# Optimization experiments

Hardware: AMD Instinct MI355X
Metric: run time of the kernel (lower is better)

Reference implementation:

```python
import math
import jax, jax.numpy as jnp
import numpy as np

D_MODEL = 256
NUM_HEADS = 8
HEAD_DIM = D_MODEL // NUM_HEADS
B, S = 4, 2048


def setup_inputs() -> dict:
    key = jax.random.key(0)
    ks = jax.random.split(key, 12)
    scale = 1.0 / math.sqrt(D_MODEL)
    inp = {
        "query": jax.random.normal(ks[0], (B, S, D_MODEL), dtype=jnp.float32),
        "key": jax.random.normal(ks[1], (B, S, D_MODEL), dtype=jnp.float32),
        "value": jax.random.normal(ks[2], (B, S, D_MODEL), dtype=jnp.float32),
        "mask": jax.random.randint(ks[3], (B, 1, S, S), 0, 2, dtype=jnp.int32),
        # nn.Linear weights are [out_features, in_features]
        "Wq": jax.random.uniform(ks[4], (D_MODEL, D_MODEL), jnp.float32, -scale, scale),
        "bq": jnp.zeros((D_MODEL,), jnp.float32),
        "Wk": jax.random.uniform(ks[5], (D_MODEL, D_MODEL), jnp.float32, -scale, scale),
        "bk": jnp.zeros((D_MODEL,), jnp.float32),
        "Wv": jax.random.uniform(ks[6], (D_MODEL, D_MODEL), jnp.float32, -scale, scale),
        "bv": jnp.zeros((D_MODEL,), jnp.float32),
        "Wo": jax.random.uniform(ks[7], (D_MODEL, D_MODEL), jnp.float32, -scale, scale),
        "bo": jnp.zeros((D_MODEL,), jnp.float32),
    }
    return inp


def _split_heads(x):
    # [B, S, d_model] -> [B, H, S, head_dim]
    b, s, _ = x.shape
    return x.reshape(b, s, NUM_HEADS, HEAD_DIM).transpose(0, 2, 1, 3)


def reference(query, key, value, mask, Wq, bq, Wk, bk, Wv, bv, Wo, bo):
    q = _split_heads(query @ Wq.T + bq)
    k = _split_heads(key @ Wk.T + bk)
    v = _split_heads(value @ Wv.T + bv)
    energy = jnp.einsum("bhqd,bhkd->bhqk", q, k)  # [B, H, S, S]
    # masked_fill(mask == 0, -inf), then scale AFTER masking (as in the source)
    energy = jnp.where(mask == 0, -jnp.inf, energy)
    attn = jax.nn.softmax(energy / math.sqrt(HEAD_DIM), axis=-1)
    out = jnp.einsum("bhqk,bhkd->bhqd", attn, v)  # [B, H, S, head_dim]
    b = out.shape[0]
    out = out.transpose(0, 2, 1, 3).reshape(b, -1, D_MODEL)
    return out @ Wo.T + bo
```

## Files before the change

### kernel.cpp

```cpp
#include <hip/hip_runtime.h>
#include <stdint.h>

#define D_MODEL 256
#define NHEAD   8
#define HDIM    32
#define BATCH   4
#define SEQ     2048
#define MTOT    (BATCH*SEQ)

typedef float f32x4 __attribute__((ext_vector_type(4)));
typedef short s16x8 __attribute__((ext_vector_type(8)));

__device__ __forceinline__ unsigned short f2bf(float f) {
    union { float f; uint32_t u; } v; v.f = f;
    uint32_t u = v.u;
    u += 0x7fffu + ((u >> 16) & 1u);
    return (unsigned short)(u >> 16);
}

__device__ __forceinline__ uint32_t cvtpk_bf16(float a, float b) {
    uint32_t r;
    asm("v_cvt_pk_bf16_f32 %0, %1, %2" : "=v"(r) : "v"(a), "v"(b));
    return r;
}

__global__ __launch_bounds__(256)
void prep(const float* __restrict__ q, const float* __restrict__ k, const float* __restrict__ v,
          const float* __restrict__ wq, const float* __restrict__ wk,
          const float* __restrict__ wv, const float* __restrict__ wo,
          unsigned short* __restrict__ qb, unsigned short* __restrict__ kb,
          unsigned short* __restrict__ vb,
          unsigned short* __restrict__ wqb, unsigned short* __restrict__ wkb,
          unsigned short* __restrict__ wvb, unsigned short* __restrict__ wob, float csc) {
    const int y = blockIdx.y;
    const float* src; unsigned short* dst; int n; float sc = 1.0f;
    switch (y) {
        case 0:  src = q;  dst = qb;  n = MTOT * 256; break;
        case 1:  src = k;  dst = kb;  n = MTOT * 256; break;
        case 2:  src = v;  dst = vb;  n = MTOT * 256; break;
        case 3:  src = wq; dst = wqb; n = 65536; sc = csc; break;
        case 4:  src = wk; dst = wkb; n = 65536; break;
        case 5:  src = wv; dst = wvb; n = 65536; break;
        default: src = wo; dst = wob; n = 65536; break;
    }
    const int i = (blockIdx.x * 256 + threadIdx.x) * 4;
    if (i >= n) return;
    f32x4 x = *(const f32x4*)(src + i);
    ushort4 o;
    o.x = f2bf(x[0] * sc); o.y = f2bf(x[1] * sc);
    o.z = f2bf(x[2] * sc); o.w = f2bf(x[3] * sc);
    *(ushort4*)(dst + i) = o;
}

__global__ void pack_mask(const int* __restrict__ mask,
                          unsigned long long* __restrict__ pm) {
    const int lane = threadIdx.x & 63;
    const int wid  = (blockIdx.x * blockDim.x + threadIdx.x) >> 6;
    const int nw   = (gridDim.x * blockDim.x) >> 6;
    const int nchunks = BATCH * SEQ * (SEQ / 64);
    for (int c = wid; c < nchunks; c += nw) {
        int v = mask[(size_t)c * 64 + lane];
        unsigned long long bits = __ballot(v != 0);
        if (lane == 0) pm[c] = bits;
    }
}

__global__ __launch_bounds__(256, 3)
void proj3(const unsigned short* __restrict__ Xq, const unsigned short* __restrict__ Xk,
           const unsigned short* __restrict__ Xv,
           const unsigned short* __restrict__ Wqb, const unsigned short* __restrict__ Wkb,
           const unsigned short* __restrict__ Wvb,
           const float* __restrict__ bq, const float* __restrict__ bk,
           const float* __restrict__ bv,
           unsigned short* __restrict__ Qh, unsigned short* __restrict__ Kh,
           unsigned short* __restrict__ Vt, float csc) {
    const int y = blockIdx.y;
    const unsigned short* X = (y == 0) ? Xq : (y == 1) ? Xk : Xv;
    const unsigned short* W = (y == 0) ? Wqb : (y == 1) ? Wkb : Wvb;
    const float* bias = (y == 0) ? bq : (y == 1) ? bk : bv;
    const float bscale = (y == 0) ? csc : 1.0f;

    const int t = threadIdx.x, lane = t & 63, w = t >> 6;
    const int fr = lane & 15, fg = lane >> 4;
    const int m0 = blockIdx.x * 32;
    const int n0w = w * 64;

    f32x4 acc[2][4] = {};

    if (y < 2) {
        #pragma unroll 2
        for (int k0 = 0; k0 < 256; k0 += 32) {
            s16x8 xf[2], wf[4];
            #pragma unroll
            for (int mg = 0; mg < 2; ++mg)
                xf[mg] = *(const s16x8*)(X + ((size_t)(m0 + mg*16 + fr) << 8) + k0 + (fg << 3));
            #pragma unroll
            for (int ng = 0; ng < 4; ++ng)
                wf[ng] = *(const s16x8*)(W + ((size_t)(n0w + ng*16 + fr) << 8) + k0 + (fg << 3));
            #pragma unroll
            for (int mg = 0; mg < 2; ++mg)
                #pragma unroll
                for (int ng = 0; ng < 4; ++ng)
                    acc[mg][ng] = __builtin_amdgcn_mfma_f32_16x16x32_bf16(
                        wf[ng], xf[mg], acc[mg][ng], 0, 0, 0);
        }
        unsigned short* OUT = (y == 0) ? Qh : Kh;
        #pragma unroll
        for (int mg = 0; mg < 2; ++mg) {
            const int m = m0 + mg*16 + fr;
            const int bb = m >> 11, ss = m & 2047;
            #pragma unroll
            for (int ng = 0; ng < 4; ++ng) {
                const int nb = n0w + ng*16 + fg*4;
                const int hh = nb >> 5, db = nb & 31;
                f32x4 bi = *(const f32x4*)(bias + nb);
                ushort4 o;
                o.x = f2bf(acc[mg][ng][0] + bi[0] * bscale);
                o.y = f2bf(acc[mg][ng][1] + bi[1] * bscale);
                o.z = f2bf(acc[mg][ng][2] + bi[2] * bscale);
                o.w = f2bf(acc[mg][ng][3] + bi[3] * bscale);
                *(ushort4*)(OUT + (((size_t)(bb*8 + hh) * SEQ) + ss) * 32 + db) = o;
            }
        }
    } else {
        #pragma unroll 2
        for (int k0 = 0; k0 < 256; k0 += 32) {
            s16x8 xf[2], wf[4];
            #pragma unroll
            for (int mg = 0; mg < 2; ++mg)
                xf[mg] = *(const s16x8*)(X + ((size_t)(m0 + mg*16 + fr) << 8) + k0 + (fg << 3));
            #pragma unroll
            for (int ng = 0; ng < 4; ++ng)
                wf[ng] = *(const s16x8*)(W + ((size_t)(n0w + ng*16 + fr) << 8) + k0 + (fg << 3));
            #pragma unroll
            for (int mg = 0; mg < 2; ++mg)
                #pragma unroll
                for (int ng = 0; ng < 4; ++ng)
                    acc[mg][ng] = __builtin_amdgcn_mfma_f32_16x16x32_bf16(
                        xf[mg], wf[ng], acc[mg][ng], 0, 0, 0);
        }
        #pragma unroll
        for (int mg = 0; mg < 2; ++mg) {
            const int sb = m0 + mg*16 + fg*4;
            const int bb = sb >> 11, ss = sb & 2047;
            #pragma unroll
            for (int ng = 0; ng < 4; ++ng) {
                const int n = n0w + ng*16 + fr;
                const int hh = n >> 5, dd = n & 31;
                const float bi = bias[n];
                ushort4 o;
                o.x = f2bf(acc[mg][ng][0] + bi);
                o.y = f2bf(acc[mg][ng][1] + bi);
                o.z = f2bf(acc[mg][ng][2] + bi);
                o.w = f2bf(acc[mg][ng][3] + bi);
                *(ushort4*)(Vt + (((size_t)(bb*8 + hh) * 32) + dd) * SEQ + ss) = o;
            }
        }
    }
}

__global__ __launch_bounds__(256, 3)
void oproj(const unsigned short* __restrict__ Ao, const unsigned short* __restrict__ Wo,
           const float* __restrict__ bo, float* __restrict__ out) {
    const int t = threadIdx.x, lane = t & 63, w = t >> 6;
    const int fr = lane & 15, fg = lane >> 4;
    const int m0 = blockIdx.x * 32;
    const int n0w = w * 64;

    f32x4 acc[2][4] = {};
    #pragma unroll 2
    for (int k0 = 0; k0 < 256; k0 += 32) {
        s16x8 xf[2], wf[4];
        #pragma unroll
        for (int mg = 0; mg < 2; ++mg)
            xf[mg] = *(const s16x8*)(Ao + ((size_t)(m0 + mg*16 + fr) << 8) + k0 + (fg << 3));
        #pragma unroll
        for (int ng = 0; ng < 4; ++ng)
            wf[ng] = *(const s16x8*)(Wo + ((size_t)(n0w + ng*16 + fr) << 8) + k0 + (fg << 3));
        #pragma unroll
        for (int mg = 0; mg < 2; ++mg)
            #pragma unroll
            for (int ng = 0; ng < 4; ++ng)
                acc[mg][ng] = __builtin_amdgcn_mfma_f32_16x16x32_bf16(
                    wf[ng], xf[mg], acc[mg][ng], 0, 0, 0);
    }
    #pragma unroll
    for (int mg = 0; mg < 2; ++mg) {
        const int m = m0 + mg*16 + fr;
        #pragma unroll
        for (int ng = 0; ng < 4; ++ng) {
            const int nb = n0w + ng*16 + fg*4;
            f32x4 bi = *(const f32x4*)(bo + nb);
            f32x4 vv = acc[mg][ng] + bi;
            *(f32x4*)(out + (size_t)m * 256 + nb) = vv;
        }
    }
}

struct TR {
    s16x8 kf[4];
    s16x8 vf[2][2];
    unsigned long long mw[2];
};

__device__ __forceinline__ void load_tile(TR& tr, int ti,
        const unsigned short* Kb, const unsigned short* Vb,
        const unsigned long long* pm0, const unsigned long long* pm1,
        int fr, int fg) {
    tr.mw[0] = pm0[ti];
    tr.mw[1] = pm1[ti];
    #pragma unroll
    for (int g = 0; g < 4; ++g)
        tr.kf[g] = *(const s16x8*)(Kb + ((ti*64 + g*16 + fr) << 5) + (fg << 3));
    #pragma unroll
    for (int c = 0; c < 2; ++c)
        #pragma unroll
        for (int hh = 0; hh < 2; ++hh)
            tr.vf[c][hh] = *(const s16x8*)(Vb + ((hh*16 + fr) << 11) + ti*64 + c*32 + (fg << 3));
}

__device__ __forceinline__ void compute_tile(const TR& tr, const s16x8* qf,
        f32x4 acc[2][2], float* mrun, float* lrun, char* ptb, int fr, int fg) {
    #pragma unroll
    for (int j = 0; j < 2; ++j) {
        const unsigned long long wsh = tr.mw[j] >> (fg * 4);
        const uint32_t wlo = (uint32_t)wsh, whi = (uint32_t)(wsh >> 32);
        f32x4 s[4];
        #pragma unroll
        for (int g = 0; g < 4; ++g) {
            const uint32_t wsel = (g < 2) ? wlo : whi;
            f32x4 cm;
            #pragma unroll
            for (int r = 0; r < 4; ++r)
                cm[r] = ((wsel >> ((g & 1) * 16 + r)) & 1u) ? 0.0f : -1.0e30f;
            s[g] = __builtin_amdgcn_mfma_f32_16x16x32_bf16(tr.kf[g], qf[j], cm, 0, 0, 0);
        }
        float v[16];
        #pragma unroll
        for (int g = 0; g < 4; ++g)
            #pragma unroll
            for (int r = 0; r < 4; ++r)
                v[g*4 + r] = s[g][r];
        float t8[8];
        #pragma unroll
        for (int i = 0; i < 8; ++i) t8[i] = fmaxf(v[2*i], v[2*i+1]);
        float mx = fmaxf(fmaxf(fmaxf(t8[0], t8[1]), fmaxf(t8[2], t8[3])),
                         fmaxf(fmaxf(t8[4], t8[5]), fmaxf(t8[6], t8[7])));
        mx = fmaxf(mx, __shfl_xor(mx, 16));
        mx = fmaxf(mx, __shfl_xor(mx, 32));
        const float mn = fmaxf(mrun[j], mx);
        const float rs = exp2f(mrun[j] - mn);
        mrun[j] = mn;
        float p[16];
        #pragma unroll
        for (int i = 0; i < 16; ++i) p[i] = exp2f(v[i] - mn);
        float s8[8];
        #pragma unroll
        for (int i = 0; i < 8; ++i) s8[i] = p[2*i] + p[2*i+1];
        float sum = ((s8[0]+s8[1]) + (s8[2]+s8[3])) + ((s8[4]+s8[5]) + (s8[6]+s8[7]));
        sum += __shfl_xor(sum, 16);
        sum += __shfl_xor(sum, 32);
        lrun[j] = lrun[j] * rs + sum;
        acc[j][0] *= rs;
        acc[j][1] *= rs;
        char* row = ptb + (j << 11) + fr * 128;
        #pragma unroll
        for (int g = 0; g < 4; ++g) {
            const uint32_t p0 = cvtpk_bf16(p[g*4+0], p[g*4+1]);
            const uint32_t p1 = cvtpk_bf16(p[g*4+2], p[g*4+3]);
            const int slot = (g*2 + (fg >> 1)) ^ (fr & 7);
            *(uint2*)(row + (slot << 4) + ((fg & 1) << 3)) = make_uint2(p0, p1);
        }
        #pragma unroll
        for (int c = 0; c < 2; ++c) {
            const int slot = (c*4 + fg) ^ (fr & 7);
            const s16x8 pb = *(const s16x8*)(row + (slot << 4));
            #pragma unroll
            for (int hh = 0; hh < 2; ++hh)
                acc[j][hh] = __builtin_amdgcn_mfma_f32_16x16x32_bf16(
                    tr.vf[c][hh], pb, acc[j][hh], 0, 0, 0);
        }
    }
}

__global__ __launch_bounds__(256, 2)
void attn_fused(const unsigned short* __restrict__ Qh,
                const unsigned short* __restrict__ Kh,
                const unsigned short* __restrict__ Vt,
                const unsigned long long* __restrict__ pm,
                unsigned short* __restrict__ Ao) {
    __shared__ __align__(16) char ptbuf[16384];
    const int t = threadIdx.x, lane = t & 63, w = t >> 6;
    const int fr = lane & 15, fg = lane >> 4;
    const int by = blockIdx.y, b = by >> 3, h = by & 7;
    const int q0 = blockIdx.x * 128 + w * 32;
    const unsigned short* Qb = Qh + (size_t)by * SEQ * HDIM;
    const unsigned short* Kb = Kh + (size_t)by * SEQ * HDIM;
    const unsigned short* Vb = Vt + (size_t)by * HDIM * SEQ;
    const unsigned long long* pm0 = pm + ((size_t)b * SEQ + q0 + fr) * 32;
    const unsigned long long* pm1 = pm0 + 16 * 32;
    char* ptb = ptbuf + (w << 12);

    s16x8 qf[2];
    #pragma unroll
    for (int j = 0; j < 2; ++j)
        qf[j] = *(const s16x8*)(Qb + ((q0 + j*16 + fr) << 5) + (fg << 3));

    f32x4 acc[2][2] = {};
    float mrun[2] = {-1e20f, -1e20f};
    float lrun[2] = {0.0f, 0.0f};

    TR A, B;
    load_tile(A, 0, Kb, Vb, pm0, pm1, fr, fg);
    #pragma unroll 1
    for (int ti = 0; ti < 32; ti += 2) {
        load_tile(B, ti + 1, Kb, Vb, pm0, pm1, fr, fg);
        compute_tile(A, qf, acc, mrun, lrun, ptb, fr, fg);
        load_tile(A, (ti + 2 < 32) ? ti + 2 : 31, Kb, Vb, pm0, pm1, fr, fg);
        compute_tile(B, qf, acc, mrun, lrun, ptb, fr, fg);
    }

    #pragma unroll
    for (int j = 0; j < 2; ++j) {
        const float inv = 1.0f / lrun[j];
        const int q = q0 + j*16 + fr;
        #pragma unroll
        for (int hh = 0; hh < 2; ++hh) {
            ushort4 o;
            o.x = f2bf(acc[j][hh][0] * inv);
            o.y = f2bf(acc[j][hh][1] * inv);
            o.z = f2bf(acc[j][hh][2] * inv);
            o.w = f2bf(acc[j][hh][3] * inv);
            *(ushort4*)(Ao + (((size_t)b * SEQ + q) * 8 + h) * 32 + hh*16 + fg*4) = o;
        }
    }
}

extern "C" void kernel_launch(void* const* d_in, const int* in_sizes, int n_in,
                              void* d_out, int out_size, void* d_ws, size_t ws_size,
                              hipStream_t stream) {
    const float* query = (const float*)d_in[0];
    const float* key   = (const float*)d_in[1];
    const float* value = (const float*)d_in[2];
    const int*   mask  = (const int*)  d_in[3];
    const float* Wq = (const float*)d_in[4];   const float* bq = (const float*)d_in[5];
    const float* Wk = (const float*)d_in[6];   const float* bk = (const float*)d_in[7];
    const float* Wv = (const float*)d_in[8];   const float* bv = (const float*)d_in[9];
    const float* Wo = (const float*)d_in[10];  const float* bo = (const float*)d_in[11];

    char* ws = (char*)d_ws;
    const size_t MB = 1024 * 1024;
    unsigned short* qbf = (unsigned short*)(ws);
    unsigned short* kbf = (unsigned short*)(ws + 4*MB);
    unsigned short* vbf = (unsigned short*)(ws + 8*MB);
    unsigned short* wqb = (unsigned short*)(ws + 12*MB);
    unsigned short* wkb = (unsigned short*)(ws + 12*MB + 131072);
    unsigned short* wvb = (unsigned short*)(ws + 12*MB + 262144);
    unsigned short* wob = (unsigned short*)(ws + 12*MB + 393216);
    unsigned long long* pmw = (unsigned long long*)(ws + 12*MB + 524288);
    unsigned short* Qh = (unsigned short*)(ws + 14*MB + 524288);
    unsigned short* Kh = (unsigned short*)(ws + 18*MB + 524288);
    unsigned short* Vt = (unsigned short*)(ws + 22*MB + 524288);
    unsigned short* Aob = (unsigned short*)(ws);

    const float csc = (float)(0.17677669529663687 * 1.4426950408889634);

    prep<<<dim3(2048, 7), 256, 0, stream>>>(query, key, value, Wq, Wk, Wv, Wo,
                                            qbf, kbf, vbf, wqb, wkb, wvb, wob, csc);
    pack_mask<<<2048, 256, 0, stream>>>(mask, pmw);
    proj3<<<dim3(256, 3), 256, 0, stream>>>(qbf, kbf, vbf, wqb, wkb, wvb,
                                            bq, bk, bv, Qh, Kh, Vt, csc);
    attn_fused<<<dim3(16, 32), 256, 0, stream>>>(Qh, Kh, Vt, pmw, Aob);
    oproj<<<dim3(256), 256, 0, stream>>>(Aob, wob, bo, (float*)d_out);
}
```

Baseline: 243.7 us.

## Fuse fp32-to-bf16 conversion into projections, split-K attention with combine, lazy rescale

The separate prep conversion kernel is removed, and the projection GEMMs now load fp32 inputs and weights and convert them to bf16 in registers. Attention is split along the key dimension into two partitions, doubling the grid. Each partition writes unnormalised fp32 partial outputs plus its running max and sum, and a new combine kernel merges them. Inside the softmax, the mask is applied after exponentiation instead of as an MFMA bias, and the online max rescale only runs when the new max exceeds the old one by more than a threshold. This trades one extra kernel and fp32 partial traffic for more parallelism and fewer full-size conversion passes, at some numerical risk from the lazy-rescale threshold.

```diff
diff --git a/kernel.cpp b/kernel.cpp
--- a/kernel.cpp
+++ b/kernel.cpp
@@ -24,32 +24,15 @@
     return r;
 }
 
-__global__ __launch_bounds__(256)
-void prep(const float* __restrict__ q, const float* __restrict__ k, const float* __restrict__ v,
-          const float* __restrict__ wq, const float* __restrict__ wk,
-          const float* __restrict__ wv, const float* __restrict__ wo,
-          unsigned short* __restrict__ qb, unsigned short* __restrict__ kb,
-          unsigned short* __restrict__ vb,
-          unsigned short* __restrict__ wqb, unsigned short* __restrict__ wkb,
-          unsigned short* __restrict__ wvb, unsigned short* __restrict__ wob, float csc) {
-    const int y = blockIdx.y;
-    const float* src; unsigned short* dst; int n; float sc = 1.0f;
-    switch (y) {
-        case 0:  src = q;  dst = qb;  n = MTOT * 256; break;
-        case 1:  src = k;  dst = kb;  n = MTOT * 256; break;
-        case 2:  src = v;  dst = vb;  n = MTOT * 256; break;
-        case 3:  src = wq; dst = wqb; n = 65536; sc = csc; break;
-        case 4:  src = wk; dst = wkb; n = 65536; break;
-        case 5:  src = wv; dst = wvb; n = 65536; break;
-        default: src = wo; dst = wob; n = 65536; break;
-    }
-    const int i = (blockIdx.x * 256 + threadIdx.x) * 4;
-    if (i >= n) return;
-    f32x4 x = *(const f32x4*)(src + i);
-    ushort4 o;
-    o.x = f2bf(x[0] * sc); o.y = f2bf(x[1] * sc);
-    o.z = f2bf(x[2] * sc); o.w = f2bf(x[3] * sc);
-    *(ushort4*)(dst + i) = o;
+__device__ __forceinline__ s16x8 ldfrag_f32(const float* p) {
+    f32x4 a = *(const f32x4*)p;
+    f32x4 b = *(const f32x4*)(p + 4);
+    union { uint32_t u[4]; s16x8 v; } r;
+    r.u[0] = cvtpk_bf16(a[0], a[1]);
+    r.u[1] = cvtpk_bf16(a[2], a[3]);
+    r.u[2] = cvtpk_bf16(b[0], b[1]);
+    r.u[3] = cvtpk_bf16(b[2], b[3]);
+    return r.v;
 }
 
 __global__ void pack_mask(const int* __restrict__ mask,
@@ -66,19 +49,19 @@
 }
 
 __global__ __launch_bounds__(256, 3)
-void proj3(const unsigned short* __restrict__ Xq, const unsigned short* __restrict__ Xk,
-           const unsigned short* __restrict__ Xv,
-           const unsigned short* __restrict__ Wqb, const unsigned short* __restrict__ Wkb,
-           const unsigned short* __restrict__ Wvb,
+void proj3(const float* __restrict__ Xq, const float* __restrict__ Xk,
+           const float* __restrict__ Xv,
+           const float* __restrict__ Wq, const float* __restrict__ Wk,
+           const float* __restrict__ Wv,
            const float* __restrict__ bq, const float* __restrict__ bk,
            const float* __restrict__ bv,
            unsigned short* __restrict__ Qh, unsigned short* __restrict__ Kh,
            unsigned short* __restrict__ Vt, float csc) {
     const int y = blockIdx.y;
-    const unsigned short* X = (y == 0) ? Xq : (y == 1) ? Xk : Xv;
-    const unsigned short* W = (y == 0) ? Wqb : (y == 1) ? Wkb : Wvb;
+    const float* X = (y == 0) ? Xq : (y == 1) ? Xk : Xv;
+    const float* W = (y == 0) ? Wq : (y == 1) ? Wk : Wv;
     const float* bias = (y == 0) ? bq : (y == 1) ? bk : bv;
-    const float bscale = (y == 0) ? csc : 1.0f;
+    const float sc = (y == 0) ? csc : 1.0f;
 
     const int t = threadIdx.x, lane = t & 63, w = t >> 6;
     const int fr = lane & 15, fg = lane >> 4;
@@ -93,10 +76,10 @@
             s16x8 xf[2], wf[4];
             #pragma unroll
             for (int mg = 0; mg < 2; ++mg)
-                xf[mg] = *(const s16x8*)(X + ((size_t)(m0 + mg*16 + fr) << 8) + k0 + (fg << 3));
+                xf[mg] = ldfrag_f32(X + ((size_t)(m0 + mg*16 + fr) << 8) + k0 + (fg << 3));
             #pragma unroll
             for (int ng = 0; ng < 4; ++ng)
-                wf[ng] = *(const s16x8*)(W + ((size_t)(n0w + ng*16 + fr) << 8) + k0 + (fg << 3));
+                wf[ng] = ldfrag_f32(W + ((size_t)(n0w + ng*16 + fr) << 8) + k0 + (fg << 3));
             #pragma unroll
             for (int mg = 0; mg < 2; ++mg)
                 #pragma unroll
@@ -115,10 +98,10 @@
                 const int hh = nb >> 5, db = nb & 31;
                 f32x4 bi = *(const f32x4*)(bias + nb);
                 ushort4 o;
-                o.x = f2bf(acc[mg][ng][0] + bi[0] * bscale);
-                o.y = f2bf(acc[mg][ng][1] + bi[1] * bscale);
-                o.z = f2bf(acc[mg][ng][2] + bi[2] * bscale);
-                o.w = f2bf(acc[mg][ng][3] + bi[3] * bscale);
+                o.x = f2bf((acc[mg][ng][0] + bi[0]) * sc);
+                o.y = f2bf((acc[mg][ng][1] + bi[1]) * sc);
+                o.z = f2bf((acc[mg][ng][2] + bi[2]) * sc);
+                o.w = f2bf((acc[mg][ng][3] + bi[3]) * sc);
                 *(ushort4*)(OUT + (((size_t)(bb*8 + hh) * SEQ) + ss) * 32 + db) = o;
             }
         }
@@ -128,10 +111,10 @@
             s16x8 xf[2], wf[4];
             #pragma unroll
             for (int mg = 0; mg < 2; ++mg)
-                xf[mg] = *(const s16x8*)(X + ((size_t)(m0 + mg*16 + fr) << 8) + k0 + (fg << 3));
+                xf[mg] = ldfrag_f32(X + ((size_t)(m0 + mg*16 + fr) << 8) + k0 + (fg << 3));
             #pragma unroll
             for (int ng = 0; ng < 4; ++ng)
-                wf[ng] = *(const s16x8*)(W + ((size_t)(n0w + ng*16 + fr) << 8) + k0 + (fg << 3));
+                wf[ng] = ldfrag_f32(W + ((size_t)(n0w + ng*16 + fr) << 8) + k0 + (fg << 3));
             #pragma unroll
             for (int mg = 0; mg < 2; ++mg)
                 #pragma unroll
@@ -160,7 +143,7 @@
 }
 
 __global__ __launch_bounds__(256, 3)
-void oproj(const unsigned short* __restrict__ Ao, const unsigned short* __restrict__ Wo,
+void oproj(const unsigned short* __restrict__ Ao, const float* __restrict__ Wo,
            const float* __restrict__ bo, float* __restrict__ out) {
     const int t = threadIdx.x, lane = t & 63, w = t >> 6;
     const int fr = lane & 15, fg = lane >> 4;
@@ -176,7 +159,7 @@
             xf[mg] = *(const s16x8*)(Ao + ((size_t)(m0 + mg*16 + fr) << 8) + k0 + (fg << 3));
         #pragma unroll
         for (int ng = 0; ng < 4; ++ng)
-            wf[ng] = *(const s16x8*)(Wo + ((size_t)(n0w + ng*16 + fr) << 8) + k0 + (fg << 3));
+            wf[ng] = ldfrag_f32(Wo + ((size_t)(n0w + ng*16 + fr) << 8) + k0 + (fg << 3));
         #pragma unroll
         for (int mg = 0; mg < 2; ++mg)
             #pragma unroll
@@ -228,12 +211,8 @@
         f32x4 s[4];
         #pragma unroll
         for (int g = 0; g < 4; ++g) {
-            const uint32_t wsel = (g < 2) ? wlo : whi;
-            f32x4 cm;
-            #pragma unroll
-            for (int r = 0; r < 4; ++r)
-                cm[r] = ((wsel >> ((g & 1) * 16 + r)) & 1u) ? 0.0f : -1.0e30f;
-            s[g] = __builtin_amdgcn_mfma_f32_16x16x32_bf16(tr.kf[g], qf[j], cm, 0, 0, 0);
+            const f32x4 cz = {0.0f, 0.0f, 0.0f, 0.0f};
+            s[g] = __builtin_amdgcn_mfma_f32_16x16x32_bf16(tr.kf[g], qf[j], cz, 0, 0, 0);
         }
         float v[16];
         #pragma unroll
@@ -241,6 +220,11 @@
             #pragma unroll
             for (int r = 0; r < 4; ++r)
                 v[g*4 + r] = s[g][r];
+
+        float p[16];
+        #pragma unroll
+        for (int i = 0; i < 16; ++i) p[i] = exp2f(v[i] - mrun[j]);
+
         float t8[8];
         #pragma unroll
         for (int i = 0; i < 8; ++i) t8[i] = fmaxf(v[2*i], v[2*i+1]);
@@ -248,21 +232,41 @@
                          fmaxf(fmaxf(t8[4], t8[5]), fmaxf(t8[6], t8[7])));
         mx = fmaxf(mx, __shfl_xor(mx, 16));
         mx = fmaxf(mx, __shfl_xor(mx, 32));
-        const float mn = fmaxf(mrun[j], mx);
-        const float rs = exp2f(mrun[j] - mn);
-        mrun[j] = mn;
-        float p[16];
-        #pragma unroll
-        for (int i = 0; i < 16; ++i) p[i] = exp2f(v[i] - mn);
+
+        #pragma unroll
+        for (int g = 0; g < 4; ++g) {
+            const uint32_t wsel = (g < 2) ? wlo : whi;
+            #pragma unroll
+            for (int r = 0; r < 4; ++r)
+                p[g*4 + r] = ((wsel >> ((g & 1) * 16 + r)) & 1u) ? p[g*4 + r] : 0.0f;
+        }
+
+        if (!__all(mx <= mrun[j] + 8.0f)) {
+            const float mn = fmaxf(mrun[j], mx);
+            const float rs = exp2f(mrun[j] - mn);
+            #pragma unroll
+            for (int i = 0; i < 16; ++i) p[i] = exp2f(v[i] - mn);
+            #pragma unroll
+            for (int g = 0; g < 4; ++g) {
+                const uint32_t wsel = (g < 2) ? wlo : whi;
+                #pragma unroll
+                for (int r = 0; r < 4; ++r)
+                    p[g*4 + r] = ((wsel >> ((g & 1) * 16 + r)) & 1u) ? p[g*4 + r] : 0.0f;
+            }
+            mrun[j] = mn;
+            lrun[j] *= rs;
+            acc[j][0] *= rs;
+            acc[j][1] *= rs;
+        }
+
         float s8[8];
         #pragma unroll
         for (int i = 0; i < 8; ++i) s8[i] = p[2*i] + p[2*i+1];
         float sum = ((s8[0]+s8[1]) + (s8[2]+s8[3])) + ((s8[4]+s8[5]) + (s8[6]+s8[7]));
         sum += __shfl_xor(sum, 16);
         sum += __shfl_xor(sum, 32);
-        lrun[j] = lrun[j] * rs + sum;
-        acc[j][0] *= rs;
-        acc[j][1] *= rs;
+        lrun[j] += sum;
+
         char* row = ptb + (j << 11) + fr * 128;
         #pragma unroll
         for (int g = 0; g < 4; ++g) {
@@ -283,21 +287,22 @@
     }
 }
 
-__global__ __launch_bounds__(256, 2)
+__global__ __launch_bounds__(256, 4)
 void attn_fused(const unsigned short* __restrict__ Qh,
                 const unsigned short* __restrict__ Kh,
                 const unsigned short* __restrict__ Vt,
                 const unsigned long long* __restrict__ pm,
-                unsigned short* __restrict__ Ao) {
+                float* __restrict__ Opart, float2* __restrict__ MLpart) {
     __shared__ __align__(16) char ptbuf[16384];
     const int t = threadIdx.x, lane = t & 63, w = t >> 6;
     const int fr = lane & 15, fg = lane >> 4;
-    const int by = blockIdx.y, b = by >> 3, h = by & 7;
+    const int by = blockIdx.y, b = by >> 3;
+    const int kz = blockIdx.z;
     const int q0 = blockIdx.x * 128 + w * 32;
     const unsigned short* Qb = Qh + (size_t)by * SEQ * HDIM;
-    const unsigned short* Kb = Kh + (size_t)by * SEQ * HDIM;
-    const unsigned short* Vb = Vt + (size_t)by * HDIM * SEQ;
-    const unsigned long long* pm0 = pm + ((size_t)b * SEQ + q0 + fr) * 32;
+    const unsigned short* Kb = Kh + (size_t)by * SEQ * HDIM + ((size_t)kz << 15);
+    const unsigned short* Vb = Vt + (size_t)by * HDIM * SEQ + ((size_t)kz << 10);
+    const unsigned long long* pm0 = pm + ((size_t)b * SEQ + q0 + fr) * 32 + kz * 16;
     const unsigned long long* pm1 = pm0 + 16 * 32;
     char* ptb = ptbuf + (w << 12);
 
@@ -313,27 +318,45 @@
     TR A, B;
     load_tile(A, 0, Kb, Vb, pm0, pm1, fr, fg);
     #pragma unroll 1
-    for (int ti = 0; ti < 32; ti += 2) {
+    for (int ti = 0; ti < 16; ti += 2) {
         load_tile(B, ti + 1, Kb, Vb, pm0, pm1, fr, fg);
         compute_tile(A, qf, acc, mrun, lrun, ptb, fr, fg);
-        load_tile(A, (ti + 2 < 32) ? ti + 2 : 31, Kb, Vb, pm0, pm1, fr, fg);
+        load_tile(A, (ti + 2 < 16) ? ti + 2 : 15, Kb, Vb, pm0, pm1, fr, fg);
         compute_tile(B, qf, acc, mrun, lrun, ptb, fr, fg);
     }
 
     #pragma unroll
     for (int j = 0; j < 2; ++j) {
-        const float inv = 1.0f / lrun[j];
         const int q = q0 + j*16 + fr;
-        #pragma unroll
-        for (int hh = 0; hh < 2; ++hh) {
-            ushort4 o;
-            o.x = f2bf(acc[j][hh][0] * inv);
-            o.y = f2bf(acc[j][hh][1] * inv);
-            o.z = f2bf(acc[j][hh][2] * inv);
-            o.w = f2bf(acc[j][hh][3] * inv);
-            *(ushort4*)(Ao + (((size_t)b * SEQ + q) * 8 + h) * 32 + hh*16 + fg*4) = o;
-        }
-    }
+        const size_t row = ((size_t)(kz*32 + by) * SEQ) + q;
+        #pragma unroll
+        for (int hh = 0; hh < 2; ++hh)
+            *(f32x4*)(Opart + row * 32 + hh*16 + fg*4) = acc[j][hh];
+        if (fg == 0)
+            MLpart[row] = make_float2(mrun[j], lrun[j]);
+    }
+}
+
+__global__ __launch_bounds__(256)
+void combine(const float* __restrict__ Opart, const float2* __restrict__ ML,
+             unsigned short* __restrict__ Ao) {
+    const int t = blockIdx.x * 256 + threadIdx.x;
+    const int row = t >> 3, c = t & 7;
+    const float2 ml1 = ML[row];
+    const float2 ml2 = ML[row + 65536];
+    const float m = fmaxf(ml1.x, ml2.x);
+    const float w1 = exp2f(ml1.x - m), w2 = exp2f(ml2.x - m);
+    const float inv = 1.0f / (w1 * ml1.y + w2 * ml2.y);
+    const f32x4 o1 = *(const f32x4*)(Opart + (size_t)row * 32 + c * 4);
+    const f32x4 o2 = *(const f32x4*)(Opart + ((size_t)row + 65536) * 32 + c * 4);
+    const int bh = row >> 11, q = row & 2047;
+    const int b = bh >> 3, h = bh & 7;
+    ushort4 o;
+    o.x = f2bf((w1 * o1[0] + w2 * o2[0]) * inv);
+    o.y = f2bf((w1 * o1[1] + w2 * o2[1]) * inv);
+    o.z = f2bf((w1 * o1[2] + w2 * o2[2]) * inv);
+    o.w = f2bf((w1 * o1[3] + w2 * o2[3]) * inv);
+    *(ushort4*)(Ao + ((size_t)(b * SEQ + q) * 256) + h * 32 + c * 4) = o;
 }
 
 extern "C" void kernel_launch(void* const* d_in, const int* in_sizes, int n_in,
@@ -350,26 +373,20 @@
 
     char* ws = (char*)d_ws;
     const size_t MB = 1024 * 1024;
-    unsigned short* qbf = (unsigned short*)(ws);
-    unsigned short* kbf = (unsigned short*)(ws + 4*MB);
-    unsigned short* vbf = (unsigned short*)(ws + 8*MB);
-    unsigned short* wqb = (unsigned short*)(ws + 12*MB);
-    unsigned short* wkb = (unsigned short*)(ws + 12*MB + 131072);
-    unsigned short* wvb = (unsigned short*)(ws + 12*MB + 262144);
-    unsigned short* wob = (unsigned short*)(ws + 12*MB + 393216);
-    unsigned long long* pmw = (unsigned long long*)(ws + 12*MB + 524288);
-    unsigned short* Qh = (unsigned short*)(ws + 14*MB + 524288);
-    unsigned short* Kh = (unsigned short*)(ws + 18*MB + 524288);
-    unsigned short* Vt = (unsigned short*)(ws + 22*MB + 524288);
-    unsigned short* Aob = (unsigned short*)(ws);
+    unsigned long long* pmw = (unsigned long long*)(ws);
+    unsigned short* Qh  = (unsigned short*)(ws + 2*MB);
+    unsigned short* Kh  = (unsigned short*)(ws + 6*MB);
+    unsigned short* Vt  = (unsigned short*)(ws + 10*MB);
+    unsigned short* Aob = (unsigned short*)(ws + 14*MB);
+    float*  Opart = (float*)(ws + 18*MB);
+    float2* MLp   = (float2*)(ws + 34*MB);
 
     const float csc = (float)(0.17677669529663687 * 1.4426950408889634);
 
-    prep<<<dim3(2048, 7), 256, 0, stream>>>(query, key, value, Wq, Wk, Wv, Wo,
-                                            qbf, kbf, vbf, wqb, wkb, wvb, wob, csc);
     pack_mask<<<2048, 256, 0, stream>>>(mask, pmw);
-    proj3<<<dim3(256, 3), 256, 0, stream>>>(qbf, kbf, vbf, wqb, wkb, wvb,
+    proj3<<<dim3(256, 3), 256, 0, stream>>>(query, key, value, Wq, Wk, Wv,
                                             bq, bk, bv, Qh, Kh, Vt, csc);
-    attn_fused<<<dim3(16, 32), 256, 0, stream>>>(Qh, Kh, Vt, pmw, Aob);
-    oproj<<<dim3(256), 256, 0, stream>>>(Aob, wob, bo, (float*)d_out);
-}
+    attn_fused<<<dim3(16, 32, 2), 256, 0, stream>>>(Qh, Kh, Vt, pmw, Opart, MLp);
+    combine<<<2048, 256, 0, stream>>>(Opart, MLp, Aob);
+    oproj<<<256, 256, 0, stream>>>(Aob, Wo, bo, (float*)d_out);
+}
```

New measurement: 340.2 us. +39.6%, slower.
